# Performance work log

Measured on AMD Instinct MI355X. Metric: run time of the kernel, lower is better.

Reference implementation:

```python
import jax, jax.numpy as jnp
import numpy as np

B, S, DIM, H, D = 2, 2048, 1024, 16, 64
WINDOW = 512
MAX_MEM_SEGMENTS = 1
ROPE_THETA = 10000.0


def _rope(t, pos):
    # lucidrains rotary-embedding-torch default: interleaved pairs
    d = t.shape[-1]
    inv_freq = 1.0 / (ROPE_THETA ** (jnp.arange(0, d, 2, dtype=jnp.float32) / d))
    freqs = pos[:, None].astype(jnp.float32) * inv_freq[None, :]        # [S, d/2]
    freqs = jnp.repeat(freqs, 2, axis=-1)                               # [S, d]
    cos, sin = jnp.cos(freqs), jnp.sin(freqs)
    t1, t2 = t[..., 0::2], t[..., 1::2]
    rot = jnp.stack((-t2, t1), axis=-1).reshape(t.shape)                # rotate_half
    return t * cos + rot * sin


def setup_inputs() -> dict:
    key = jax.random.key(0)
    ks = jax.random.split(key, 8)
    tokens = jax.random.normal(ks[0], (B, S, DIM), dtype=jnp.float32)
    value_residual = jax.random.normal(ks[1], (B, H, S, D), dtype=jnp.float32)
    episode_ids = jnp.sort(jax.random.randint(ks[2], (B, S), 0, 4), axis=-1)
    w = 0.02
    Wq = jax.random.normal(ks[3], (DIM, H * D), dtype=jnp.float32) * w
    Wkv = jax.random.normal(ks[4], (DIM, 2 * H * D), dtype=jnp.float32) * w
    Wo = jax.random.normal(ks[5], (H * D, DIM), dtype=jnp.float32) * w
    Wg = jax.random.normal(ks[6], (DIM, H), dtype=jnp.float32) * w
    Wmix = jax.random.normal(ks[7], (DIM, H), dtype=jnp.float32) * w
    return {"tokens": tokens, "value_residual": value_residual, "episode_ids": episode_ids,
            "Wq": Wq, "Wkv": Wkv, "Wo": Wo, "Wg": Wg, "Wmix": Wmix}


def reference(tokens, value_residual, episode_ids, Wq, Wkv, Wo, Wg, Wmix):
    b, s, _ = tokens.shape
    scale = D ** -0.5

    def split_heads(x):  # [b, n, h*d] -> [b, h, n, d]
        return x.reshape(b, s, H, D).transpose(0, 2, 1, 3)

    q = split_heads(tokens @ Wq)
    kv = tokens @ Wkv
    k, v = split_heads(kv[..., :H * D]), split_heads(kv[..., H * D:])

    q = q * scale

    # value-residual lerp: v.lerp(value_residual, mix)
    mix = jax.nn.sigmoid(jnp.einsum('bnd,dh->bhn', tokens, Wmix))[..., None]  # [b,h,n,1]
    v = v + mix * (value_residual - v)

    pos = jnp.arange(s)
    q = _rope(q, pos)
    k = _rope(k, pos)

    sim = jnp.einsum('bhid,bhjd->bhij', q, k)

    # fixed-window causal mask: masked where dist < 0 or dist > max_mem_segments*window
    dist = pos[:, None] - pos[None, :]
    win_mask = (dist < 0) | (dist > MAX_MEM_SEGMENTS * WINDOW)            # [s, s]
    ep_mask = episode_ids[:, :, None] != episode_ids[:, None, :]          # [b, s, s]
    mask = win_mask[None, None, :, :] | ep_mask[:, None, :, :]

    sim = jnp.where(mask, -jnp.finfo(sim.dtype).max, sim)
    attn = jax.nn.softmax(sim, axis=-1)
    out = jnp.einsum('bhij,bhjd->bhid', attn, v)

    # sigmoid value gating
    gate = jax.nn.sigmoid(jnp.einsum('bnd,dh->bhn', tokens, Wg))[..., None]
    out = out * gate

    out = out.transpose(0, 2, 1, 3).reshape(b, s, H * D)
    return out @ Wo
```

## Files before the change

### kernel.cpp

```cpp
#include <hip/hip_runtime.h>
#include <math.h>

#define BB 2
#define SS 2048
#define DIMM 1024
#define HH 16
#define DD 64
#define WINDOW 512

typedef __bf16 bf16x8 __attribute__((ext_vector_type(8)));
typedef float f32x4 __attribute__((ext_vector_type(4)));

__device__ __forceinline__ unsigned short f2bf(float f) {
    unsigned int u = __float_as_uint(f);
    u = (u + 0x7FFFu + ((u >> 16) & 1u)) >> 16;
    return (unsigned short)u;
}
__device__ __forceinline__ float bf2f(unsigned short u) {
    return __uint_as_float((unsigned int)u << 16);
}

__device__ __forceinline__ void async_cp16(unsigned short* lds_dst, const unsigned short* g_src) {
    __builtin_amdgcn_global_load_lds(
        (const __attribute__((address_space(1))) unsigned int*)g_src,
        (__attribute__((address_space(3))) unsigned int*)lds_dst, 16, 0, 0);
}

__global__ __launch_bounds__(256) void prep_kernel(
    const float* __restrict__ tokens, unsigned short* __restrict__ tokA,
    const float* __restrict__ Wg, const float* __restrict__ Wmix,
    unsigned short* __restrict__ wgmt,
    const int* __restrict__ ep, int* __restrict__ epstart)
{
    int bid = blockIdx.x;
    int tid = threadIdx.x;
    if (bid < 2048) {
        const int n4 = (BB * SS * DIMM) / 4;
        for (int i = bid * 256 + tid; i < n4; i += 2048 * 256) {
            float4 v = ((const float4*)tokens)[i];
            ushort4 o;
            o.x = f2bf(v.x); o.y = f2bf(v.y); o.z = f2bf(v.z); o.w = f2bf(v.w);
            ((ushort4*)tokA)[i] = o;
        }
    } else if (bid < 2176) {
        int idx = (bid - 2048) * 256 + tid;
        int n = idx >> 10, k = idx & 1023;
        const float* src = (n < 16) ? Wg : Wmix;
        wgmt[idx] = f2bf(src[k * HH + (n & 15)]);
    } else {
        int idx = (bid - 2176) * 256 + tid;
        int b = idx >> 11, i = idx & 2047;
        const int* e = ep + b * SS;
        int v = e[i];
        int lo = 0, hi = i;
        while (lo < hi) {
            int mid = (lo + hi) >> 1;
            if (e[mid] == v) hi = mid; else lo = mid + 1;
        }
        epstart[idx] = lo;
    }
}

__global__ __launch_bounds__(256) void transpose_cvt3_kernel(
    const float* __restrict__ Wq, const float* __restrict__ Wkv,
    const float* __restrict__ Wo, unsigned short* __restrict__ BtW,
    unsigned short* __restrict__ WotW)
{
    int z = blockIdx.z;
    const float* src = (z == 0) ? Wq : (z == 1) ? Wkv : Wo;
    unsigned short* dst = (z == 0) ? BtW : (z == 1) ? (BtW + 1024 * 1024) : WotW;
    int C = (z == 1) ? 2048 : 1024;
    if (blockIdx.x * 32 >= C) return;
    const int R = 1024;

    __shared__ float t[32][33];
    int c0 = blockIdx.x * 32, r0 = blockIdx.y * 32;
    int tx = threadIdx.x & 31, ty = threadIdx.x >> 5;
    #pragma unroll
    for (int u = 0; u < 4; ++u)
        t[ty + 8 * u][tx] = src[(size_t)(r0 + ty + 8 * u) * C + c0 + tx];
    __syncthreads();
    #pragma unroll
    for (int u = 0; u < 4; ++u)
        dst[(size_t)(c0 + ty + 8 * u) * R + r0 + tx] = f2bf(t[tx][ty + 8 * u]);
}

__global__ __launch_bounds__(256) void mixgate_mfma(
    const unsigned short* __restrict__ A,
    const unsigned short* __restrict__ Bt,
    float* __restrict__ gate, float* __restrict__ mix)
{
    int mbase = blockIdx.x * 16;
    int tid = threadIdx.x;
    int wave = tid >> 6, lane = tid & 63;
    int fr = lane & 15, hi = lane >> 4;
    int kw = wave * 256;

    __shared__ float red[4][16][32];

    f32x4 acc[2];
    acc[0] = (f32x4){0.f, 0.f, 0.f, 0.f};
    acc[1] = (f32x4){0.f, 0.f, 0.f, 0.f};

    const unsigned short* a0 = A + (size_t)(mbase + fr) * 1024 + kw + hi * 8;
    const unsigned short* b0 = Bt + (size_t)fr * 1024 + kw + hi * 8;
    const unsigned short* b1 = Bt + (size_t)(16 + fr) * 1024 + kw + hi * 8;

    #pragma unroll 2
    for (int k = 0; k < 256; k += 32) {
        bf16x8 af0 = *(const bf16x8*)(a0 + k);
        bf16x8 bf0 = *(const bf16x8*)(b0 + k);
        bf16x8 bf1 = *(const bf16x8*)(b1 + k);
        acc[0] = __builtin_amdgcn_mfma_f32_16x16x32_bf16(af0, bf0, acc[0], 0, 0, 0);
        acc[1] = __builtin_amdgcn_mfma_f32_16x16x32_bf16(af0, bf1, acc[1], 0, 0, 0);
    }

    #pragma unroll
    for (int n_ = 0; n_ < 2; ++n_)
        #pragma unroll
        for (int j = 0; j < 4; ++j)
            red[wave][hi * 4 + j][n_ * 16 + fr] = acc[n_][j];
    __syncthreads();

    #pragma unroll
    for (int e = 0; e < 2; ++e) {
        int idx = tid * 2 + e;
        int r = idx >> 5, c = idx & 31;
        float s4 = red[0][r][c] + red[1][r][c] + red[2][r][c] + red[3][r][c];
        float sg = 1.f / (1.f + __expf(-s4));
        int mg = mbase + r;
        int b = mg >> 11, s = mg & 2047;
        int h = c & 15;
        float* dst = (c < 16) ? gate : mix;
        dst[((size_t)b * HH + h) * SS + s] = sg;
    }
}

template<int EPI, int BM, int BN>
__global__ __launch_bounds__(256) void gemm_mfma(
    const unsigned short* __restrict__ A, const unsigned short* __restrict__ Bt,
    void* __restrict__ o0v, void* __restrict__ o1v, void* __restrict__ o2v)
{
    const int K = 1024;
    constexpr int MFR = BM / 32;
    constexpr int NFR = BN / 32;
    int nbase = blockIdx.x * BN;
    int mbase = blockIdx.y * BM;

    int tid = threadIdx.x;
    int lane = tid & 63;
    int wave = tid >> 6;
    int wr = wave >> 1, wc = wave & 1;
    int fr = lane & 15, hi = lane >> 4;

    __shared__ unsigned short As[2][BM * 32];
    __shared__ unsigned short Bs[2][BN * 32];

    int srow = tid >> 2;
    int sp   = tid & 3;
    int scol = (sp ^ ((srow >> 1) & 3)) * 8;
    const unsigned short* agp0 = A  + (size_t)(mbase + srow) * K + scol;
    const unsigned short* agp1 = (BM == 128)
        ? A + (size_t)(mbase + srow + 64) * K + scol : agp0;
    const unsigned short* bgp0 = Bt + (size_t)(nbase + srow) * K + scol;
    const unsigned short* bgp1 = (BN == 128)
        ? Bt + (size_t)(nbase + srow + 64) * K + scol : bgp0;

    f32x4 acc[MFR][NFR];
    #pragma unroll
    for (int m_ = 0; m_ < MFR; ++m_)
        #pragma unroll
        for (int n_ = 0; n_ < NFR; ++n_)
            acc[m_][n_] = (f32x4){0.f, 0.f, 0.f, 0.f};

    int aidx[MFR], bidx[NFR];
    #pragma unroll
    for (int m_ = 0; m_ < MFR; ++m_) {
        int row = wr * (BM / 2) + m_ * 16 + fr;
        aidx[m_] = row * 32 + (hi ^ ((row >> 1) & 3)) * 8;
    }
    #pragma unroll
    for (int n_ = 0; n_ < NFR; ++n_) {
        int row = wc * (BN / 2) + n_ * 16 + fr;
        bidx[n_] = row * 32 + (hi ^ ((row >> 1) & 3)) * 8;
    }

    auto stage = [&](int buf, int k0) {
        async_cp16(&As[buf][tid * 8], agp0 + k0);
        if constexpr (BM == 128)
            async_cp16(&As[buf][2048 + tid * 8], agp1 + k0);
        async_cp16(&Bs[buf][tid * 8], bgp0 + k0);
        if constexpr (BN == 128)
            async_cp16(&Bs[buf][2048 + tid * 8], bgp1 + k0);
    };

    stage(0, 0);
    for (int k0 = 0; k0 < K; k0 += 32) {
        int cur = (k0 >> 5) & 1;
        __syncthreads();
        if (k0 + 32 < K) stage(cur ^ 1, k0 + 32);

        bf16x8 af[MFR], bfr[NFR];
        #pragma unroll
        for (int m_ = 0; m_ < MFR; ++m_) af[m_] = *(const bf16x8*)&As[cur][aidx[m_]];
        #pragma unroll
        for (int n_ = 0; n_ < NFR; ++n_) bfr[n_] = *(const bf16x8*)&Bs[cur][bidx[n_]];
        #pragma unroll
        for (int m_ = 0; m_ < MFR; ++m_)
            #pragma unroll
            for (int n_ = 0; n_ < NFR; ++n_)
                acc[m_][n_] = __builtin_amdgcn_mfma_f32_16x16x32_bf16(
                    af[m_], bfr[n_], acc[m_][n_], 0, 0, 0);
    }

    #pragma unroll
    for (int m_ = 0; m_ < MFR; ++m_) {
        #pragma unroll
        for (int n_ = 0; n_ < NFR; ++n_) {
            int c = nbase + wc * (BN / 2) + n_ * 16 + fr;
            #pragma unroll
            for (int j = 0; j < 4; ++j) {
                int mg = mbase + wr * (BM / 2) + m_ * 16 + hi * 4 + j;
                float v = acc[m_][n_][j];
                if (EPI == 0) {
                    ((float*)o0v)[(size_t)mg * 1024 + c] = v;
                } else {
                    int b = mg >> 11, s = mg & 2047;
                    int cc = c & 1023, h = cc >> 6, d = cc & 63;
                    unsigned short* dst = (c < 1024) ? (unsigned short*)o0v
                                        : (c < 2048) ? (unsigned short*)o1v
                                                     : (unsigned short*)o2v;
                    dst[(((size_t)b * HH + h) * SS + s) * DD + d] = f2bf(v);
                }
            }
        }
    }
}

__global__ __launch_bounds__(256) void rope_lerp_kernel(
    unsigned short* __restrict__ q, unsigned short* __restrict__ k,
    const unsigned short* __restrict__ v0, const float* __restrict__ vres,
    const float* __restrict__ mix, unsigned short* __restrict__ vt)
{
    int st = blockIdx.x;
    int bh = blockIdx.y;
    int tid = threadIdx.x;
    int sl = tid >> 2;
    int dg = (tid & 3) * 16;
    int s = st * 64 + sl;
    size_t rowoff = ((size_t)bh * SS + s) * DD + dg;

    __shared__ unsigned short vtile[64][66];

    union { uint4 v[2]; unsigned short u[16]; } qa, ka, va;
    qa.v[0] = *(const uint4*)(q + rowoff);
    qa.v[1] = *(const uint4*)(q + rowoff + 8);
    ka.v[0] = *(const uint4*)(k + rowoff);
    ka.v[1] = *(const uint4*)(k + rowoff + 8);
    va.v[0] = *(const uint4*)(v0 + rowoff);
    va.v[1] = *(const uint4*)(v0 + rowoff + 8);
    float4 w[4];
    #pragma unroll
    for (int u = 0; u < 4; ++u) w[u] = *(const float4*)(vres + rowoff + 4 * u);
    float mx = mix[(size_t)bh * SS + s];

    #pragma unroll
    for (int u = 0; u < 8; ++u) {
        int d0 = dg + 2 * u;
        float inv_freq = powf(10000.f, -(float)d0 * (1.f / 64.f));
        float fr = (float)s * inv_freq;
        float red = fr - 6.2831853f * floorf(fr * 0.15915494f);
        float cs, sn;
        __sincosf(red, &sn, &cs);
        float x = bf2f(qa.u[2 * u]), y = bf2f(qa.u[2 * u + 1]);
        qa.u[2 * u]     = f2bf((x * cs - y * sn) * 0.125f);
        qa.u[2 * u + 1] = f2bf((y * cs + x * sn) * 0.125f);
        x = bf2f(ka.u[2 * u]); y = bf2f(ka.u[2 * u + 1]);
        ka.u[2 * u]     = f2bf(x * cs - y * sn);
        ka.u[2 * u + 1] = f2bf(y * cs + x * sn);
    }
    *(uint4*)(q + rowoff)     = qa.v[0];
    *(uint4*)(q + rowoff + 8) = qa.v[1];
    *(uint4*)(k + rowoff)     = ka.v[0];
    *(uint4*)(k + rowoff + 8) = ka.v[1];

    #pragma unroll
    for (int e = 0; e < 16; ++e) {
        float vv = bf2f(va.u[e]);
        float wr = ((const float*)w)[e];
        vtile[sl][dg + e] = f2bf(vv + mx * (wr - vv));
    }
    __syncthreads();

    int d = tid >> 2;
    int sseg = (tid & 3) * 16;
    union { uint4 v[2]; unsigned short u[16]; } ot;
    #pragma unroll
    for (int e = 0; e < 16; ++e) ot.u[e] = vtile[sseg + e][d];
    unsigned short* dst = vt + ((size_t)bh * DD + d) * SS + st * 64 + sseg;
    *(uint4*)dst = ot.v[0];
    *(uint4*)(dst + 8) = ot.v[1];
}

__global__ __launch_bounds__(256) void attn_mfma(
    const unsigned short* __restrict__ qbh, const unsigned short* __restrict__ kbh,
    const unsigned short* __restrict__ vt, const int* __restrict__ epstart,
    const float* __restrict__ gate, unsigned short* __restrict__ ao)
{
    int orig = blockIdx.x;
    int swz  = (orig & 7) * 128 + (orig >> 3);
    int bh = swz >> 5, qt = swz & 31;
    int b = bh >> 4, h = bh & 15;
    int q0 = qt * 64;
    int tid = threadIdx.x;
    int wave = tid >> 6, lane = tid & 63;
    int lq = lane & 15, lg = lane >> 4;
    int i = q0 + wave * 16 + lq;

    __shared__ unsigned short Ks[3][4096];
    __shared__ unsigned short Vs[3][4096];
    alignas(16) __shared__ unsigned short P_lds[4][16][72];

    int srow0 = tid >> 3, sch = tid & 7;
    int srow1 = srow0 + 32;
    int sc0 = ((sch ^ (srow0 & 7)) << 3);
    int sc1 = ((sch ^ (srow1 & 7)) << 3);
    const unsigned short* kS0 = kbh + ((size_t)bh * SS + srow0) * DD + sc0;
    const unsigned short* kS1 = kbh + ((size_t)bh * SS + srow1) * DD + sc1;
    const unsigned short* vS0 = vt + ((size_t)bh * DD + srow0) * SS + sc0;
    const unsigned short* vS1 = vt + ((size_t)bh * DD + srow1) * SS + sc1;

    auto stageKV = [&](int buf, int jbase) {
        async_cp16(&Ks[buf][tid * 8],        kS0 + (size_t)jbase * DD);
        async_cp16(&Ks[buf][2048 + tid * 8], kS1 + (size_t)jbase * DD);
        async_cp16(&Vs[buf][tid * 8],        vS0 + jbase);
        async_cp16(&Vs[buf][2048 + tid * 8], vS1 + jbase);
    };

    int fidx[4];
    #pragma unroll
    for (int n = 0; n < 4; ++n) {
        int r = 16 * n + lq;
        fidx[n] = r * 64 + ((lg ^ (r & 7)) << 3);
    }

    const unsigned short* qrow = qbh + ((size_t)bh * SS + i) * DD + lg * 8;
    bf16x8 bq0 = *(const bf16x8*)qrow;
    bf16x8 bq1 = *(const bf16x8*)(qrow + 32);

    int jmin = i - WINDOW;
    int es = epstart[b * SS + i];
    if (es > jmin) jmin = es;
    float gi = gate[(size_t)bh * SS + i];

    float m = -1e30f, l = 0.f;
    f32x4 o[4];
    #pragma unroll
    for (int n = 0; n < 4; ++n) o[n] = (f32x4){0.f, 0.f, 0.f, 0.f};

    int t0 = (qt < 8) ? (8 - qt) : 0;
    int nt = 9 - t0;
    int jb0 = 64 * (qt - 8 + t0);

    stageKV(0, jb0);
    if (nt > 1) stageKV(1, jb0 + 64);

    for (int u = 0; u < nt; ++u) {
        if (u + 1 < nt) asm volatile("s_waitcnt vmcnt(4)" ::: "memory");
        else            asm volatile("s_waitcnt vmcnt(0)" ::: "memory");
        __builtin_amdgcn_s_barrier();
        if (u + 2 < nt) stageKV((u + 2) % 3, jb0 + 64 * (u + 2));
        int buf = u % 3;
        int jbase = jb0 + 64 * u;

        f32x4 acc[4];
        #pragma unroll
        for (int n = 0; n < 4; ++n) acc[n] = (f32x4){0.f, 0.f, 0.f, 0.f};
        #pragma unroll
        for (int n = 0; n < 4; ++n) {
            bf16x8 kf0 = *(const bf16x8*)&Ks[buf][fidx[n]];
            bf16x8 kf1 = *(const bf16x8*)&Ks[buf][fidx[n] ^ 32];
            acc[n] = __builtin_amdgcn_mfma_f32_16x16x32_bf16(kf0, bq0, acc[n], 0, 0, 0);
            acc[n] = __builtin_amdgcn_mfma_f32_16x16x32_bf16(kf1, bq1, acc[n], 0, 0, 0);
        }

        int jb = jbase + lg * 4;
        #pragma unroll
        for (int n = 0; n < 4; ++n)
            #pragma unroll
            for (int r = 0; r < 4; ++r) {
                int j = jb + 16 * n + r;
                if (j < jmin || j > i) acc[n][r] = -3e38f;
            }

        float tm = -3e38f;
        #pragma unroll
        for (int n = 0; n < 4; ++n)
            tm = fmaxf(tm, fmaxf(fmaxf(acc[n][0], acc[n][1]), fmaxf(acc[n][2], acc[n][3])));
        tm = fmaxf(tm, __shfl_xor(tm, 16, 64));
        tm = fmaxf(tm, __shfl_xor(tm, 32, 64));
        float mnew = fmaxf(m, tm);
        float scale = __expf(m - mnew);
        float ts = 0.f;
        #pragma unroll
        for (int n = 0; n < 4; ++n)
            #pragma unroll
            for (int r = 0; r < 4; ++r) {
                float p = __expf(acc[n][r] - mnew);
                acc[n][r] = p;
                ts += p;
            }
        ts += __shfl_xor(ts, 16, 64);
        ts += __shfl_xor(ts, 32, 64);
        l = l * scale + ts;
        m = mnew;
        #pragma unroll
        for (int n = 0; n < 4; ++n) o[n] = o[n] * scale;

        #pragma unroll
        for (int n = 0; n < 4; ++n) {
            ushort4 u4;
            u4.x = f2bf(acc[n][0]); u4.y = f2bf(acc[n][1]);
            u4.z = f2bf(acc[n][2]); u4.w = f2bf(acc[n][3]);
            *(ushort4*)&P_lds[wave][lq][16 * n + lg * 4] = u4;
        }
        bf16x8 bp0 = *(const bf16x8*)&P_lds[wave][lq][lg * 8];
        bf16x8 bp1 = *(const bf16x8*)&P_lds[wave][lq][32 + lg * 8];

        #pragma unroll
        for (int n = 0; n < 4; ++n) {
            bf16x8 vf0 = *(const bf16x8*)&Vs[buf][fidx[n]];
            bf16x8 vf1 = *(const bf16x8*)&Vs[buf][fidx[n] ^ 32];
            o[n] = __builtin_amdgcn_mfma_f32_16x16x32_bf16(vf0, bp0, o[n], 0, 0, 0);
            o[n] = __builtin_amdgcn_mfma_f32_16x16x32_bf16(vf1, bp1, o[n], 0, 0, 0);
        }
    }

    float g = gi / l;
    #pragma unroll
    for (int n = 0; n < 4; ++n) {
        ushort4 u4;
        u4.x = f2bf(o[n][0] * g); u4.y = f2bf(o[n][1] * g);
        u4.z = f2bf(o[n][2] * g); u4.w = f2bf(o[n][3] * g);
        *(ushort4*)(ao + (((size_t)b * SS + i) * HH + h) * DD + 16 * n + lg * 4) = u4;
    }
}

extern "C" void kernel_launch(void* const* d_in, const int* in_sizes, int n_in,
                              void* d_out, int out_size, void* d_ws, size_t ws_size,
                              hipStream_t stream)
{
    const float* tokens = (const float*)d_in[0];
    const float* vres   = (const float*)d_in[1];
    const int*   ep     = (const int*)d_in[2];
    const float* Wq     = (const float*)d_in[3];
    const float* Wkv    = (const float*)d_in[4];
    const float* Wo     = (const float*)d_in[5];
    const float* Wg     = (const float*)d_in[6];
    const float* Wmix   = (const float*)d_in[7];
    float* out = (float*)d_out;

    char* wsb = (char*)d_ws;
    unsigned short* qbh  = (unsigned short*)(wsb + 0);
    unsigned short* kbh  = (unsigned short*)(wsb + 8388608);
    unsigned short* vb0  = (unsigned short*)(wsb + 16777216);
    unsigned short* vtb  = (unsigned short*)(wsb + 25165824);
    unsigned short* aob  = (unsigned short*)(wsb + 33554432);
    unsigned short* tokA = (unsigned short*)(wsb + 41943040);
    unsigned short* BtW  = (unsigned short*)(wsb + 50331648);
    float* gatep = (float*)(wsb + 56623104);
    float* mixp  = (float*)(wsb + 56885248);
    int*   epst  = (int*)(wsb + 57147392);
    unsigned short* wgmt = (unsigned short*)(wsb + 57163776);
    unsigned short* WotW = (unsigned short*)(wsb + 57229312);

    prep_kernel<<<2192, 256, 0, stream>>>(tokens, tokA, Wg, Wmix, wgmt, ep, epst);
    transpose_cvt3_kernel<<<dim3(64, 32, 3), 256, 0, stream>>>(Wq, Wkv, Wo, BtW, WotW);

    mixgate_mfma<<<256, 256, 0, stream>>>(tokA, wgmt, gatep, mixp);
    gemm_mfma<1, 128, 128><<<dim3(24, 32), 256, 0, stream>>>(tokA, BtW, qbh, kbh, vb0);
    rope_lerp_kernel<<<dim3(SS / 64, BB * HH), 256, 0, stream>>>(qbh, kbh, vb0, vres, mixp, vtb);
    attn_mfma<<<1024, 256, 0, stream>>>(qbh, kbh, vtb, epst, gatep, aob);

    gemm_mfma<0, 128, 64><<<dim3(16, 32), 256, 0, stream>>>(aob, WotW, out, nullptr, nullptr);
}
```

Before: 126.7 us.

## Single-buffer K/V staging in attention with wave priority and native bf16 casts

Replaces the three-stage asynchronous K/V prefetch ring with one LDS buffer that is loaded and fenced by barriers on every tile. This cuts LDS per block roughly threefold, so more blocks can be resident, at the cost of no longer overlapping loads with MFMA work. It also raises wave priority around the MFMA sections with s_setprio. Manual bit-twiddled float-to-bf16 rounding is replaced by native __bf16 casts, which the compiler may lower to hardware convert instructions.

```diff
diff --git a/kernel.cpp b/kernel.cpp
--- a/kernel.cpp
+++ b/kernel.cpp
@@ -9,6 +9,7 @@
 #define WINDOW 512
 
 typedef __bf16 bf16x8 __attribute__((ext_vector_type(8)));
+typedef __bf16 bf16x4 __attribute__((ext_vector_type(4)));
 typedef float f32x4 __attribute__((ext_vector_type(4)));
 
 __device__ __forceinline__ unsigned short f2bf(float f) {
@@ -317,8 +318,8 @@
     int lq = lane & 15, lg = lane >> 4;
     int i = q0 + wave * 16 + lq;
 
-    __shared__ unsigned short Ks[3][4096];
-    __shared__ unsigned short Vs[3][4096];
+    __shared__ unsigned short Ks[4096];
+    __shared__ unsigned short Vs[4096];
     alignas(16) __shared__ unsigned short P_lds[4][16][72];
 
     int srow0 = tid >> 3, sch = tid & 7;
@@ -330,13 +331,6 @@
     const unsigned short* vS0 = vt + ((size_t)bh * DD + srow0) * SS + sc0;
     const unsigned short* vS1 = vt + ((size_t)bh * DD + srow1) * SS + sc1;
 
-    auto stageKV = [&](int buf, int jbase) {
-        async_cp16(&Ks[buf][tid * 8],        kS0 + (size_t)jbase * DD);
-        async_cp16(&Ks[buf][2048 + tid * 8], kS1 + (size_t)jbase * DD);
-        async_cp16(&Vs[buf][tid * 8],        vS0 + jbase);
-        async_cp16(&Vs[buf][2048 + tid * 8], vS1 + jbase);
-    };
-
     int fidx[4];
     #pragma unroll
     for (int n = 0; n < 4; ++n) {
@@ -362,27 +356,28 @@
     int nt = 9 - t0;
     int jb0 = 64 * (qt - 8 + t0);
 
-    stageKV(0, jb0);
-    if (nt > 1) stageKV(1, jb0 + 64);
-
     for (int u = 0; u < nt; ++u) {
-        if (u + 1 < nt) asm volatile("s_waitcnt vmcnt(4)" ::: "memory");
-        else            asm volatile("s_waitcnt vmcnt(0)" ::: "memory");
-        __builtin_amdgcn_s_barrier();
-        if (u + 2 < nt) stageKV((u + 2) % 3, jb0 + 64 * (u + 2));
-        int buf = u % 3;
         int jbase = jb0 + 64 * u;
 
+        __syncthreads();
+        async_cp16(&Ks[tid * 8],        kS0 + (size_t)jbase * DD);
+        async_cp16(&Ks[2048 + tid * 8], kS1 + (size_t)jbase * DD);
+        async_cp16(&Vs[tid * 8],        vS0 + jbase);
+        async_cp16(&Vs[2048 + tid * 8], vS1 + jbase);
+        __syncthreads();
+
         f32x4 acc[4];
         #pragma unroll
         for (int n = 0; n < 4; ++n) acc[n] = (f32x4){0.f, 0.f, 0.f, 0.f};
+        __builtin_amdgcn_s_setprio(1);
         #pragma unroll
         for (int n = 0; n < 4; ++n) {
-            bf16x8 kf0 = *(const bf16x8*)&Ks[buf][fidx[n]];
-            bf16x8 kf1 = *(const bf16x8*)&Ks[buf][fidx[n] ^ 32];
+            bf16x8 kf0 = *(const bf16x8*)&Ks[fidx[n]];
+            bf16x8 kf1 = *(const bf16x8*)&Ks[fidx[n] ^ 32];
             acc[n] = __builtin_amdgcn_mfma_f32_16x16x32_bf16(kf0, bq0, acc[n], 0, 0, 0);
             acc[n] = __builtin_amdgcn_mfma_f32_16x16x32_bf16(kf1, bq1, acc[n], 0, 0, 0);
         }
+        __builtin_amdgcn_s_setprio(0);
 
         int jb = jbase + lg * 4;
         #pragma unroll
@@ -419,30 +414,32 @@
 
         #pragma unroll
         for (int n = 0; n < 4; ++n) {
-            ushort4 u4;
-            u4.x = f2bf(acc[n][0]); u4.y = f2bf(acc[n][1]);
-            u4.z = f2bf(acc[n][2]); u4.w = f2bf(acc[n][3]);
-            *(ushort4*)&P_lds[wave][lq][16 * n + lg * 4] = u4;
+            bf16x4 pv;
+            pv[0] = (__bf16)acc[n][0]; pv[1] = (__bf16)acc[n][1];
+            pv[2] = (__bf16)acc[n][2]; pv[3] = (__bf16)acc[n][3];
+            *(bf16x4*)&P_lds[wave][lq][16 * n + lg * 4] = pv;
         }
         bf16x8 bp0 = *(const bf16x8*)&P_lds[wave][lq][lg * 8];
         bf16x8 bp1 = *(const bf16x8*)&P_lds[wave][lq][32 + lg * 8];
 
+        __builtin_amdgcn_s_setprio(1);
         #pragma unroll
         for (int n = 0; n < 4; ++n) {
-            bf16x8 vf0 = *(const bf16x8*)&Vs[buf][fidx[n]];
-            bf16x8 vf1 = *(const bf16x8*)&Vs[buf][fidx[n] ^ 32];
+            bf16x8 vf0 = *(const bf16x8*)&Vs[fidx[n]];
+            bf16x8 vf1 = *(const bf16x8*)&Vs[fidx[n] ^ 32];
             o[n] = __builtin_amdgcn_mfma_f32_16x16x32_bf16(vf0, bp0, o[n], 0, 0, 0);
             o[n] = __builtin_amdgcn_mfma_f32_16x16x32_bf16(vf1, bp1, o[n], 0, 0, 0);
         }
+        __builtin_amdgcn_s_setprio(0);
     }
 
     float g = gi / l;
     #pragma unroll
     for (int n = 0; n < 4; ++n) {
-        ushort4 u4;
-        u4.x = f2bf(o[n][0] * g); u4.y = f2bf(o[n][1] * g);
-        u4.z = f2bf(o[n][2] * g); u4.w = f2bf(o[n][3] * g);
-        *(ushort4*)(ao + (((size_t)b * SS + i) * HH + h) * DD + 16 * n + lg * 4) = u4;
+        bf16x4 ov;
+        ov[0] = (__bf16)(o[n][0] * g); ov[1] = (__bf16)(o[n][1] * g);
+        ov[2] = (__bf16)(o[n][2] * g); ov[3] = (__bf16)(o[n][3] * g);
+        *(bf16x4*)(ao + (((size_t)b * SS + i) * HH + h) * DD + 16 * n + lg * 4) = ov;
     }
 }
 
```

After: 117.8 us. -7.0%, faster.
